# Kernel optimization log

Measured on AMD Instinct MI355X. Metric: run time of the kernel, lower is better.

## Reference

```python
import jax, jax.numpy as jnp
import numpy as np

B, S, D, H = 4, 2048, 1024, 16
DH = D // H  # 64


def setup_inputs() -> dict:
    key = jax.random.key(0)
    ks = jax.random.split(key, 11)
    s = 0.02
    return {
        "query": jax.random.normal(ks[0], (B, S, D), jnp.float32),
        "key": jax.random.normal(ks[1], (B, S, D), jnp.float32),
        "value": jax.random.normal(ks[2], (B, S, D), jnp.float32),
        "Wq": jax.random.normal(ks[3], (D, D), jnp.float32) * s,
        "bq": jnp.zeros((D,), jnp.float32),
        "Wk": jax.random.normal(ks[4], (D, D), jnp.float32) * s,
        "bk": jnp.zeros((D,), jnp.float32),
        "Wv": jax.random.normal(ks[5], (D, D), jnp.float32) * s,
        "bv": jnp.zeros((D,), jnp.float32),
        "Wo": jax.random.normal(ks[6], (D, D), jnp.float32) * s,
        "bo": jnp.zeros((D,), jnp.float32),
    }


def reference(query, key, value, Wq, bq, Wk, bk, Wv, bv, Wo, bo):
    b, s, _ = query.shape
    # linear projections (torch Linear: x @ W^T + b; here W stored as [in, out])
    q = query @ Wq + bq
    k = key @ Wk + bk
    v = value @ Wv + bv
    # split heads -> [B, H, S, DH]
    q = q.reshape(b, s, H, DH).transpose(0, 2, 1, 3)
    k = k.reshape(b, s, H, DH).transpose(0, 2, 1, 3)
    v = v.reshape(b, s, H, DH).transpose(0, 2, 1, 3)
    scale = jnp.sqrt(jnp.asarray(DH, jnp.float32))
    attn = jnp.einsum("bhqd,bhkd->bhqk", q, k) / scale  # [B,H,S,S]
    attn = jax.nn.softmax(attn, axis=-1)
    out = jnp.einsum("bhqk,bhkd->bhqd", attn, v)
    out = out.transpose(0, 2, 1, 3).reshape(b, s, D)
    return out @ Wo + bo
```

## Files before the change

kernel.cpp:

```cpp
#include <hip/hip_runtime.h>

typedef float f32x4 __attribute__((ext_vector_type(4)));
typedef __bf16 bf16x8 __attribute__((ext_vector_type(8)));
typedef unsigned short u16;
typedef unsigned int u32;
typedef u16 u16x4 __attribute__((ext_vector_type(4)));
typedef u16 u16x8 __attribute__((ext_vector_type(8)));
typedef u32 u32x2 __attribute__((ext_vector_type(2)));
typedef u32 u32x4 __attribute__((ext_vector_type(4)));

constexpr int Bn = 4, Sn = 2048, Dn = 1024, Hn = 16, DHn = 64;
constexpr int Mn = Bn * Sn;

static __device__ __forceinline__ u16 f2bf(float f) {
  return __builtin_bit_cast(u16, (__bf16)f);
}

static __device__ __forceinline__ u32 cvtpk(float lo, float hi) {
  u32 r;
  asm("v_cvt_pk_bf16_f32 %0, %1, %2" : "=v"(r) : "v"(lo), "v"(hi));
  return r;
}

static __device__ __forceinline__ void async16(const void* g, void* l) {
  __builtin_amdgcn_global_load_lds((const __attribute__((address_space(1))) u32*)g,
                                   (__attribute__((address_space(3))) u32*)l, 16, 0, 0);
}

static __device__ __forceinline__ void wait_bar2() {
  asm volatile("s_waitcnt vmcnt(2)" ::: "memory");
  __builtin_amdgcn_sched_barrier(0);
  __builtin_amdgcn_s_barrier();
  __builtin_amdgcn_sched_barrier(0);
}
static __device__ __forceinline__ void wait_bar0() {
  asm volatile("s_waitcnt vmcnt(0)" ::: "memory");
  __builtin_amdgcn_sched_barrier(0);
  __builtin_amdgcn_s_barrier();
  __builtin_amdgcn_sched_barrier(0);
}
static __device__ __forceinline__ void wait_bar8() {
  asm volatile("s_waitcnt vmcnt(8)" ::: "memory");
  __builtin_amdgcn_sched_barrier(0);
  __builtin_amdgcn_s_barrier();
  __builtin_amdgcn_sched_barrier(0);
}
static __device__ __forceinline__ void raw_bar() {
  __builtin_amdgcn_sched_barrier(0);
  __builtin_amdgcn_s_barrier();
  __builtin_amdgcn_sched_barrier(0);
}

__global__ void __launch_bounds__(256) cvt3_kernel(const float* __restrict__ q,
                                                   const float* __restrict__ k,
                                                   const float* __restrict__ v,
                                                   u16* __restrict__ dst) {
  const int i = blockIdx.x * 256 + threadIdx.x;
  const int t = i >> 20;
  const int li = i & 1048575;
  const float* s = (t == 0) ? q : (t == 1) ? k : v;
  const f32x4* sp = (const f32x4*)s + (size_t)li * 2;
  const f32x4 a = sp[0], b = sp[1];
  u16x8 o;
  o[0] = f2bf(a[0]); o[1] = f2bf(a[1]); o[2] = f2bf(a[2]); o[3] = f2bf(a[3]);
  o[4] = f2bf(b[0]); o[5] = f2bf(b[1]); o[6] = f2bf(b[2]); o[7] = f2bf(b[3]);
  ((u16x8*)dst)[i] = o;
}

__global__ void __launch_bounds__(256) transpose_w_kernel(const float* __restrict__ W,
                                                          u16* __restrict__ Wt) {
  __shared__ float tile[32][33];
  const int n0 = blockIdx.x * 32, k0 = blockIdx.y * 32;
  const int tx = threadIdx.x & 31, ty = (threadIdx.x >> 5) * 4;
#pragma unroll
  for (int i = 0; i < 4; ++i)
    tile[ty + i][tx] = W[(size_t)(k0 + ty + i) * Dn + n0 + tx];
  __syncthreads();
#pragma unroll
  for (int i = 0; i < 4; ++i)
    Wt[(size_t)(n0 + ty + i) * Dn + k0 + tx] = f2bf(tile[tx][ty + i]);
}

template <int MODE>
__global__ void __launch_bounds__(256) gemm_kernel(const u16* __restrict__ A,
                                                   const u16* __restrict__ Bt,
                                                   const float* __restrict__ bias,
                                                   void* __restrict__ outp, float scale) {
  __shared__ u16 As[2][128 * 64];
  __shared__ u16 Bs[2][128 * 64];
  const int tid = threadIdx.x;
  const int wave = tid >> 6, lane = tid & 63;
  const int g = lane >> 4, c = lane & 15;
  const int m0 = blockIdx.y * 128, n0 = blockIdx.x * 128;
  const int wm = wave >> 1, wn = wave & 1;
  const int srow = lane >> 3, blk = lane & 7;

  f32x4 acc[4][4] = {};
  constexpr int NK = Dn / 64;

#pragma unroll
  for (int p = 0; p < 2; ++p) {
    const int k0 = p * 64;
#pragma unroll
    for (int i = 0; i < 4; ++i) {
      const int ch = wave * 4 + i;
      const int row = ch * 8 + srow;
      const int sblk = blk ^ srow;
      async16(A + (size_t)(m0 + row) * Dn + k0 + sblk * 8, As[p] + ch * 512);
      async16(Bt + (size_t)(n0 + row) * Dn + k0 + sblk * 8, Bs[p] + ch * 512);
    }
  }

  for (int k = 0; k < NK; ++k) {
    const int cur = k & 1;
    if (k + 1 < NK) wait_bar8(); else wait_bar0();

#pragma unroll
    for (int kk = 0; kk < 2; ++kk) {
      bf16x8 af[4], bfr[4];
#pragma unroll
      for (int mi = 0; mi < 4; ++mi)
        af[mi] = *(const bf16x8*)(As[cur] + (wm * 64 + mi * 16 + c) * 64 +
                                  (((kk * 4 + g) ^ (c & 7)) * 8));
#pragma unroll
      for (int ni = 0; ni < 4; ++ni)
        bfr[ni] = *(const bf16x8*)(Bs[cur] + (wn * 64 + ni * 16 + c) * 64 +
                                   (((kk * 4 + g) ^ (c & 7)) * 8));
#pragma unroll
      for (int mi = 0; mi < 4; ++mi)
#pragma unroll
        for (int ni = 0; ni < 4; ++ni)
          acc[mi][ni] = __builtin_amdgcn_mfma_f32_16x16x32_bf16(af[mi], bfr[ni],
                                                                acc[mi][ni], 0, 0, 0);
    }

    raw_bar();
    if (k + 2 < NK) {
      const int k0 = (k + 2) * 64;
#pragma unroll
      for (int i = 0; i < 4; ++i) {
        const int ch = wave * 4 + i;
        const int row = ch * 8 + srow;
        const int sblk = blk ^ srow;
        async16(A + (size_t)(m0 + row) * Dn + k0 + sblk * 8, As[cur] + ch * 512);
        async16(Bt + (size_t)(n0 + row) * Dn + k0 + sblk * 8, Bs[cur] + ch * 512);
      }
    }
  }

#pragma unroll
  for (int ni = 0; ni < 4; ++ni) {
    const int col = n0 + wn * 64 + ni * 16 + c;
    const float bv = bias[col];
#pragma unroll
    for (int mi = 0; mi < 4; ++mi) {
      const int row = m0 + wm * 64 + mi * 16 + g * 4;
      if constexpr (MODE == 0) {
        const int hh = col >> 6, dh = col & 63;
        const int bb = row >> 11, s = row & 2047;
        u16* o = (u16*)outp + (((size_t)(bb * Hn + hh) * Sn + s) * DHn + dh);
#pragma unroll
        for (int r = 0; r < 4; ++r)
          o[(size_t)r * DHn] = f2bf((acc[mi][ni][r] + bv) * scale);
      } else if constexpr (MODE == 1) {
        const int hh = col >> 6, dh = col & 63;
        const int bb = row >> 11, s = row & 2047;
        u16x4 pk;
#pragma unroll
        for (int r = 0; r < 4; ++r) pk[r] = f2bf(acc[mi][ni][r] + bv);
        *(u16x4*)((u16*)outp + ((size_t)(bb * Hn + hh) * DHn + dh) * Sn + s) = pk;
      } else {
        float* o = (float*)outp + (size_t)row * Dn + col;
#pragma unroll
        for (int r = 0; r < 4; ++r) o[(size_t)r * Dn] = acc[mi][ni][r] + bv;
      }
    }
  }
}

__global__ void __launch_bounds__(512, 4) attn_kernel(const u16* __restrict__ Q,
                                                      const u16* __restrict__ Kp,
                                                      const u16* __restrict__ VT,
                                                      u16* __restrict__ O) {
  __shared__ u16 Ks[3][64 * 64];
  __shared__ u16 Vs[3][64 * 64];
  const int tid = threadIdx.x;
  const int wave = tid >> 6, lane = tid & 63;
  const int g = lane >> 4, c = lane & 15;
  const int bh = blockIdx.x;
  const int q0 = blockIdx.y * 256 + wave * 32;
  const u16* Qb = Q + (size_t)bh * Sn * DHn;
  const u16* Kb = Kp + (size_t)bh * Sn * DHn;
  const u16* Vb = VT + (size_t)bh * DHn * Sn;

  bf16x8 qf[2][2];
#pragma unroll
  for (int fq = 0; fq < 2; ++fq)
#pragma unroll
    for (int kk = 0; kk < 2; ++kk)
      qf[fq][kk] = *(const bf16x8*)(Qb + (size_t)(q0 + fq * 16 + c) * DHn + kk * 32 + g * 8);

  f32x4 ot[4][2] = {};
  f32x4 lacc[2] = {};
  u16x8 one8u;
#pragma unroll
  for (int j = 0; j < 8; ++j) one8u[j] = 0x3F80;
  const bf16x8 one8 = __builtin_bit_cast(bf16x8, one8u);
  const f32x4 zf = {};

  const int srow = lane >> 3, blk = lane & 7;
  const int krow = wave * 8 + srow;
  const int sblk = blk ^ srow;
  constexpr int NT = Sn / 64;

  u16 *kA = Ks[0], *kB = Ks[1], *kC = Ks[2];
  u16 *vA = Vs[0], *vB = Vs[1], *vC = Vs[2];

#pragma unroll
  for (int tt = 0; tt < 2; ++tt) {
    const int kt = tt * 64;
    async16(Kb + (size_t)(kt + krow) * DHn + sblk * 8, Ks[tt] + wave * 512);
    async16(Vb + (size_t)krow * Sn + kt + sblk * 8, Vs[tt] + wave * 512);
  }

  for (int t = 0; t < NT; ++t) {
    if (t + 1 < NT) wait_bar2(); else wait_bar0();

    if (t + 2 < NT) {
      const int kt = (t + 2) * 64;
      async16(Kb + (size_t)(kt + krow) * DHn + sblk * 8, kC + wave * 512);
      async16(Vb + (size_t)krow * Sn + kt + sblk * 8, vC + wave * 512);
    }

    f32x4 st[4][2];
    {
      bf16x8 kf[4];
#pragma unroll
      for (int fk = 0; fk < 4; ++fk)
        kf[fk] = *(const bf16x8*)(kA + (fk * 16 + c) * 64 + ((g ^ (c & 7)) * 8));
      __builtin_amdgcn_s_setprio(1);
#pragma unroll
      for (int fk = 0; fk < 4; ++fk)
#pragma unroll
        for (int fq = 0; fq < 2; ++fq)
          st[fk][fq] = __builtin_amdgcn_mfma_f32_16x16x32_bf16(kf[fk], qf[fq][0],
                                                               zf, 0, 0, 0);
      __builtin_amdgcn_s_setprio(0);
#pragma unroll
      for (int fk = 0; fk < 4; ++fk)
        kf[fk] = *(const bf16x8*)(kA + (fk * 16 + c) * 64 + (((4 + g) ^ (c & 7)) * 8));
      __builtin_amdgcn_s_setprio(1);
#pragma unroll
      for (int fk = 0; fk < 4; ++fk)
#pragma unroll
        for (int fq = 0; fq < 2; ++fq)
          st[fk][fq] = __builtin_amdgcn_mfma_f32_16x16x32_bf16(kf[fk], qf[fq][1],
                                                               st[fk][fq], 0, 0, 0);
      __builtin_amdgcn_s_setprio(0);
    }

#pragma unroll
    for (int fq = 0; fq < 2; ++fq)
#pragma unroll
      for (int fk = 0; fk < 4; ++fk)
#pragma unroll
        for (int r = 0; r < 4; ++r)
          st[fk][fq][r] = __builtin_amdgcn_exp2f(st[fk][fq][r]);

    bf16x8 pf[2][2];
#pragma unroll
    for (int fq = 0; fq < 2; ++fq)
#pragma unroll
      for (int kk = 0; kk < 2; ++kk) {
        u32x4 pw;
#pragma unroll
        for (int w = 0; w < 2; ++w) {
          const u32 a = cvtpk(st[2 * kk][fq][2 * w], st[2 * kk][fq][2 * w + 1]);
          const u32 b = cvtpk(st[2 * kk + 1][fq][2 * w], st[2 * kk + 1][fq][2 * w + 1]);
          const u32x2 p1 = __builtin_amdgcn_permlane32_swap(a, b, false, false);
          const u32x2 p2 = __builtin_amdgcn_permlane16_swap(p1[0], p1[1], false, false);
          pw[w] = p2[0];
          pw[2 + w] = p2[1];
        }
        pf[kk][fq] = __builtin_bit_cast(bf16x8, pw);
      }

#pragma unroll
    for (int kk = 0; kk < 2; ++kk) {
      bf16x8 vf[4];
#pragma unroll
      for (int fa = 0; fa < 4; ++fa)
        vf[fa] = *(const bf16x8*)(vA + (fa * 16 + c) * 64 +
                                  (((kk * 4 + g) ^ (c & 7)) * 8));
      __builtin_amdgcn_s_setprio(1);
#pragma unroll
      for (int fa = 0; fa < 4; ++fa)
#pragma unroll
        for (int fq = 0; fq < 2; ++fq)
          ot[fa][fq] = __builtin_amdgcn_mfma_f32_16x16x32_bf16(vf[fa], pf[kk][fq],
                                                               ot[fa][fq], 0, 0, 0);
#pragma unroll
      for (int fq = 0; fq < 2; ++fq)
        lacc[fq] = __builtin_amdgcn_mfma_f32_16x16x32_bf16(one8, pf[kk][fq],
                                                           lacc[fq], 0, 0, 0);
      __builtin_amdgcn_s_setprio(0);
    }

    u16* tk = kA; kA = kB; kB = kC; kC = tk;
    u16* tv = vA; vA = vB; vB = vC; vC = tv;
  }

  const int bb = bh >> 4, hh = bh & 15;
#pragma unroll
  for (int fq = 0; fq < 2; ++fq) {
    const float inv = 1.f / lacc[fq][0];
    const int s = q0 + fq * 16 + c;
#pragma unroll
    for (int fa = 0; fa < 4; ++fa) {
      const int dh = fa * 16 + g * 4;
      u16x4 pk;
#pragma unroll
      for (int r = 0; r < 4; ++r) pk[r] = f2bf(ot[fa][fq][r] * inv);
      *(u16x4*)(O + ((size_t)bb * Sn + s) * Dn + hh * 64 + dh) = pk;
    }
  }
}

extern "C" void kernel_launch(void* const* d_in, const int* in_sizes, int n_in,
                              void* d_out, int out_size, void* d_ws, size_t ws_size,
                              hipStream_t stream) {
  (void)in_sizes; (void)n_in; (void)out_size; (void)ws_size;
  const float* q_in = (const float*)d_in[0];
  const float* k_in = (const float*)d_in[1];
  const float* v_in = (const float*)d_in[2];
  const float* Wq = (const float*)d_in[3];
  const float* bq = (const float*)d_in[4];
  const float* Wk = (const float*)d_in[5];
  const float* bk = (const float*)d_in[6];
  const float* Wv = (const float*)d_in[7];
  const float* bv = (const float*)d_in[8];
  const float* Wo = (const float*)d_in[9];
  const float* bo = (const float*)d_in[10];

  char* ws = (char*)d_ws;
  const size_t szX = (size_t)Mn * Dn * 2;
  const size_t szW = (size_t)Dn * Dn * 2;
  u16* Xq = (u16*)(ws + 0 * szX);
  u16* Xk = (u16*)(ws + 1 * szX);
  u16* Xv = (u16*)(ws + 2 * szX);
  u16* Wqt = (u16*)(ws + 3 * szX + 0 * szW);
  u16* Wkt = (u16*)(ws + 3 * szX + 1 * szW);
  u16* Wvt = (u16*)(ws + 3 * szX + 2 * szW);
  u16* Wot = (u16*)(ws + 3 * szX + 3 * szW);
  u16* Qb = (u16*)(ws + 3 * szX + 4 * szW + 0 * szX);
  u16* Kb = (u16*)(ws + 3 * szX + 4 * szW + 1 * szX);
  u16* VTb = (u16*)(ws + 3 * szX + 4 * szW + 2 * szX);
  u16* Ob = (u16*)(ws + 3 * szX + 4 * szW + 3 * szX);

  cvt3_kernel<<<3 * Mn * Dn / 8 / 256, 256, 0, stream>>>(q_in, k_in, v_in, Xq);

  dim3 tg(32, 32);
  transpose_w_kernel<<<tg, 256, 0, stream>>>(Wq, Wqt);
  transpose_w_kernel<<<tg, 256, 0, stream>>>(Wk, Wkt);
  transpose_w_kernel<<<tg, 256, 0, stream>>>(Wv, Wvt);
  transpose_w_kernel<<<tg, 256, 0, stream>>>(Wo, Wot);

  dim3 gg(Dn / 128, Mn / 128);
  const float qscale = 0.125f * 1.4426950408889634f;
  gemm_kernel<0><<<gg, 256, 0, stream>>>(Xq, Wqt, bq, Qb, qscale);
  gemm_kernel<0><<<gg, 256, 0, stream>>>(Xk, Wkt, bk, Kb, 1.0f);
  gemm_kernel<1><<<gg, 256, 0, stream>>>(Xv, Wvt, bv, VTb, 1.0f);

  attn_kernel<<<dim3(Bn * Hn, Sn / 256), 512, 0, stream>>>(Qb, Kb, VTb, Ob);

  gemm_kernel<2><<<gg, 256, 0, stream>>>(Ob, Wot, bo, d_out, 1.0f);
}
```

Baseline: 204.4 us.

## Fuse fp32-to-bf16 input conversion into batched QKV GEMM; merge weight transposes

Removes the separate cvt3 kernel that wrote bf16 copies of query/key/value. The QKV GEMM now loads fp32 activations into registers, converts them to bf16 and writes them to LDS, while B tiles still arrive via async global-to-LDS loads. The three projection GEMMs and the four weight transposes are each merged into one launch using blockIdx.z. This saves a full bf16 round trip through memory and several launches, but the GEMM now reads twice as many activation bytes and uses register-staged A loads, which may hurt overlap.

```diff
diff --git a/kernel.cpp b/kernel.cpp
--- a/kernel.cpp
+++ b/kernel.cpp
@@ -33,43 +33,45 @@
   __builtin_amdgcn_s_barrier();
   __builtin_amdgcn_sched_barrier(0);
 }
+static __device__ __forceinline__ void wait_bar4() {
+  asm volatile("s_waitcnt vmcnt(4)" ::: "memory");
+  __builtin_amdgcn_sched_barrier(0);
+  __builtin_amdgcn_s_barrier();
+  __builtin_amdgcn_sched_barrier(0);
+}
+static __device__ __forceinline__ void wait_bar8() {
+  asm volatile("s_waitcnt vmcnt(8)" ::: "memory");
+  __builtin_amdgcn_sched_barrier(0);
+  __builtin_amdgcn_s_barrier();
+  __builtin_amdgcn_sched_barrier(0);
+}
 static __device__ __forceinline__ void wait_bar0() {
   asm volatile("s_waitcnt vmcnt(0)" ::: "memory");
   __builtin_amdgcn_sched_barrier(0);
   __builtin_amdgcn_s_barrier();
   __builtin_amdgcn_sched_barrier(0);
 }
-static __device__ __forceinline__ void wait_bar8() {
-  asm volatile("s_waitcnt vmcnt(8)" ::: "memory");
-  __builtin_amdgcn_sched_barrier(0);
-  __builtin_amdgcn_s_barrier();
-  __builtin_amdgcn_sched_barrier(0);
-}
 static __device__ __forceinline__ void raw_bar() {
   __builtin_amdgcn_sched_barrier(0);
   __builtin_amdgcn_s_barrier();
   __builtin_amdgcn_sched_barrier(0);
 }
-
-__global__ void __launch_bounds__(256) cvt3_kernel(const float* __restrict__ q,
-                                                   const float* __restrict__ k,
-                                                   const float* __restrict__ v,
-                                                   u16* __restrict__ dst) {
-  const int i = blockIdx.x * 256 + threadIdx.x;
-  const int t = i >> 20;
-  const int li = i & 1048575;
-  const float* s = (t == 0) ? q : (t == 1) ? k : v;
-  const f32x4* sp = (const f32x4*)s + (size_t)li * 2;
-  const f32x4 a = sp[0], b = sp[1];
-  u16x8 o;
-  o[0] = f2bf(a[0]); o[1] = f2bf(a[1]); o[2] = f2bf(a[2]); o[3] = f2bf(a[3]);
-  o[4] = f2bf(b[0]); o[5] = f2bf(b[1]); o[6] = f2bf(b[2]); o[7] = f2bf(b[3]);
-  ((u16x8*)dst)[i] = o;
-}
-
-__global__ void __launch_bounds__(256) transpose_w_kernel(const float* __restrict__ W,
-                                                          u16* __restrict__ Wt) {
+static __device__ __forceinline__ void lgkm_bar() {
+  asm volatile("s_waitcnt lgkmcnt(0)" ::: "memory");
+  __builtin_amdgcn_sched_barrier(0);
+  __builtin_amdgcn_s_barrier();
+  __builtin_amdgcn_sched_barrier(0);
+}
+
+__global__ void __launch_bounds__(256) transpose4_kernel(const float* __restrict__ Wq,
+                                                         const float* __restrict__ Wk,
+                                                         const float* __restrict__ Wv,
+                                                         const float* __restrict__ Wo,
+                                                         u16* __restrict__ Wts) {
   __shared__ float tile[32][33];
+  const int z = blockIdx.z;
+  const float* W = (z == 0) ? Wq : (z == 1) ? Wk : (z == 2) ? Wv : Wo;
+  u16* Wt = Wts + (size_t)z * Dn * Dn;
   const int n0 = blockIdx.x * 32, k0 = blockIdx.y * 32;
   const int tx = threadIdx.x & 31, ty = (threadIdx.x >> 5) * 4;
 #pragma unroll
@@ -81,11 +83,135 @@
     Wt[(size_t)(n0 + ty + i) * Dn + k0 + tx] = f2bf(tile[tx][ty + i]);
 }
 
-template <int MODE>
-__global__ void __launch_bounds__(256) gemm_kernel(const u16* __restrict__ A,
-                                                   const u16* __restrict__ Bt,
-                                                   const float* __restrict__ bias,
-                                                   void* __restrict__ outp, float scale) {
+__global__ void __launch_bounds__(256) gemm_qkv_kernel(const float* __restrict__ q_in,
+                                                       const float* __restrict__ k_in,
+                                                       const float* __restrict__ v_in,
+                                                       const u16* __restrict__ Wts,
+                                                       const float* __restrict__ bq,
+                                                       const float* __restrict__ bk,
+                                                       const float* __restrict__ bv,
+                                                       u16* __restrict__ outbase) {
+  __shared__ u16 As[2][128 * 64];
+  __shared__ u16 Bs[2][128 * 64];
+  const int z = blockIdx.z;
+  const float* A = (z == 0) ? q_in : (z == 1) ? k_in : v_in;
+  const u16* Bt = Wts + (size_t)z * Dn * Dn;
+  const float* bias = (z == 0) ? bq : (z == 1) ? bk : bv;
+  u16* outp = outbase + (size_t)z * Mn * Dn;
+  const float scale = (z == 0) ? 0.125f * 1.4426950408889634f : 1.0f;
+
+  const int tid = threadIdx.x;
+  const int wave = tid >> 6, lane = tid & 63;
+  const int g = lane >> 4, c = lane & 15;
+  const int m0 = blockIdx.y * 128, n0 = blockIdx.x * 128;
+  const int wm = wave >> 1, wn = wave & 1;
+  const int srow = lane >> 3, blk = lane & 7;
+
+  f32x4 acc[4][4] = {};
+  constexpr int NK = Dn / 64;
+
+  f32x4 ralo[4], rahi[4];
+
+  auto issueA = [&](int k0) {
+#pragma unroll
+    for (int i = 0; i < 4; ++i) {
+      const int row = (wave * 4 + i) * 8 + srow;
+      const float* src = A + (size_t)(m0 + row) * Dn + k0 + blk * 8;
+      ralo[i] = *(const f32x4*)src;
+      rahi[i] = *(const f32x4*)(src + 4);
+    }
+  };
+  auto writeA = [&](u16* dst) {
+#pragma unroll
+    for (int i = 0; i < 4; ++i) {
+      const int row = (wave * 4 + i) * 8 + srow;
+      u32x4 w;
+      w[0] = cvtpk(ralo[i][0], ralo[i][1]);
+      w[1] = cvtpk(ralo[i][2], ralo[i][3]);
+      w[2] = cvtpk(rahi[i][0], rahi[i][1]);
+      w[3] = cvtpk(rahi[i][2], rahi[i][3]);
+      *(u32x4*)(dst + row * 64 + ((blk ^ srow) * 8)) = w;
+    }
+  };
+  auto issueB = [&](int k0, u16* dstB) {
+#pragma unroll
+    for (int i = 0; i < 4; ++i) {
+      const int ch = wave * 4 + i, row = ch * 8 + srow, sb = blk ^ srow;
+      async16(Bt + (size_t)(n0 + row) * Dn + k0 + sb * 8, dstB + ch * 512);
+    }
+  };
+
+  issueA(0);
+  issueB(0, Bs[0]);
+  asm volatile("s_waitcnt vmcnt(4)" ::: "memory");
+  __builtin_amdgcn_sched_barrier(0);
+  writeA(As[0]);
+  issueA(64);
+  issueB(64, Bs[1]);
+  asm volatile("s_waitcnt lgkmcnt(0)" ::: "memory");
+  __builtin_amdgcn_sched_barrier(0);
+
+  for (int k = 0; k < NK; ++k) {
+    const int cur = k & 1;
+    if (k + 1 < NK) wait_bar4(); else wait_bar0();
+
+    if (k + 1 < NK) writeA(As[cur ^ 1]);
+
+#pragma unroll
+    for (int kk = 0; kk < 2; ++kk) {
+      bf16x8 af[4], bfr[4];
+#pragma unroll
+      for (int mi = 0; mi < 4; ++mi)
+        af[mi] = *(const bf16x8*)(As[cur] + (wm * 64 + mi * 16 + c) * 64 +
+                                  (((kk * 4 + g) ^ (c & 7)) * 8));
+#pragma unroll
+      for (int ni = 0; ni < 4; ++ni)
+        bfr[ni] = *(const bf16x8*)(Bs[cur] + (wn * 64 + ni * 16 + c) * 64 +
+                                   (((kk * 4 + g) ^ (c & 7)) * 8));
+#pragma unroll
+      for (int mi = 0; mi < 4; ++mi)
+#pragma unroll
+        for (int ni = 0; ni < 4; ++ni)
+          acc[mi][ni] = __builtin_amdgcn_mfma_f32_16x16x32_bf16(af[mi], bfr[ni],
+                                                                acc[mi][ni], 0, 0, 0);
+    }
+
+    lgkm_bar();
+    if (k + 2 < NK) {
+      issueA((k + 2) * 64);
+      issueB((k + 2) * 64, Bs[cur]);
+    }
+  }
+
+  const bool vmode = (z == 2);
+#pragma unroll
+  for (int ni = 0; ni < 4; ++ni) {
+    const int col = n0 + wn * 64 + ni * 16 + c;
+    const float bv = bias[col];
+    const int hh = col >> 6, dh = col & 63;
+#pragma unroll
+    for (int mi = 0; mi < 4; ++mi) {
+      const int row = m0 + wm * 64 + mi * 16 + g * 4;
+      const int bb = row >> 11, s = row & 2047;
+      if (!vmode) {
+        u16* o = outp + (((size_t)(bb * Hn + hh) * Sn + s) * DHn + dh);
+#pragma unroll
+        for (int r = 0; r < 4; ++r)
+          o[(size_t)r * DHn] = f2bf((acc[mi][ni][r] + bv) * scale);
+      } else {
+        u16x4 pk;
+#pragma unroll
+        for (int r = 0; r < 4; ++r) pk[r] = f2bf(acc[mi][ni][r] + bv);
+        *(u16x4*)(outp + ((size_t)(bb * Hn + hh) * DHn + dh) * Sn + s) = pk;
+      }
+    }
+  }
+}
+
+__global__ void __launch_bounds__(256) gemm_o_kernel(const u16* __restrict__ A,
+                                                     const u16* __restrict__ Bt,
+                                                     const float* __restrict__ bias,
+                                                     float* __restrict__ outp) {
   __shared__ u16 As[2][128 * 64];
   __shared__ u16 Bs[2][128 * 64];
   const int tid = threadIdx.x;
@@ -155,25 +281,9 @@
 #pragma unroll
     for (int mi = 0; mi < 4; ++mi) {
       const int row = m0 + wm * 64 + mi * 16 + g * 4;
-      if constexpr (MODE == 0) {
-        const int hh = col >> 6, dh = col & 63;
-        const int bb = row >> 11, s = row & 2047;
-        u16* o = (u16*)outp + (((size_t)(bb * Hn + hh) * Sn + s) * DHn + dh);
-#pragma unroll
-        for (int r = 0; r < 4; ++r)
-          o[(size_t)r * DHn] = f2bf((acc[mi][ni][r] + bv) * scale);
-      } else if constexpr (MODE == 1) {
-        const int hh = col >> 6, dh = col & 63;
-        const int bb = row >> 11, s = row & 2047;
-        u16x4 pk;
-#pragma unroll
-        for (int r = 0; r < 4; ++r) pk[r] = f2bf(acc[mi][ni][r] + bv);
-        *(u16x4*)((u16*)outp + ((size_t)(bb * Hn + hh) * DHn + dh) * Sn + s) = pk;
-      } else {
-        float* o = (float*)outp + (size_t)row * Dn + col;
-#pragma unroll
-        for (int r = 0; r < 4; ++r) o[(size_t)r * Dn] = acc[mi][ni][r] + bv;
-      }
+      float* o = outp + (size_t)row * Dn + col;
+#pragma unroll
+      for (int r = 0; r < 4; ++r) o[(size_t)r * Dn] = acc[mi][ni][r] + bv;
     }
   }
 }
@@ -345,33 +455,19 @@
   char* ws = (char*)d_ws;
   const size_t szX = (size_t)Mn * Dn * 2;
   const size_t szW = (size_t)Dn * Dn * 2;
-  u16* Xq = (u16*)(ws + 0 * szX);
-  u16* Xk = (u16*)(ws + 1 * szX);
-  u16* Xv = (u16*)(ws + 2 * szX);
-  u16* Wqt = (u16*)(ws + 3 * szX + 0 * szW);
-  u16* Wkt = (u16*)(ws + 3 * szX + 1 * szW);
-  u16* Wvt = (u16*)(ws + 3 * szX + 2 * szW);
-  u16* Wot = (u16*)(ws + 3 * szX + 3 * szW);
-  u16* Qb = (u16*)(ws + 3 * szX + 4 * szW + 0 * szX);
-  u16* Kb = (u16*)(ws + 3 * szX + 4 * szW + 1 * szX);
-  u16* VTb = (u16*)(ws + 3 * szX + 4 * szW + 2 * szX);
-  u16* Ob = (u16*)(ws + 3 * szX + 4 * szW + 3 * szX);
-
-  cvt3_kernel<<<3 * Mn * Dn / 8 / 256, 256, 0, stream>>>(q_in, k_in, v_in, Xq);
-
-  dim3 tg(32, 32);
-  transpose_w_kernel<<<tg, 256, 0, stream>>>(Wq, Wqt);
-  transpose_w_kernel<<<tg, 256, 0, stream>>>(Wk, Wkt);
-  transpose_w_kernel<<<tg, 256, 0, stream>>>(Wv, Wvt);
-  transpose_w_kernel<<<tg, 256, 0, stream>>>(Wo, Wot);
-
-  dim3 gg(Dn / 128, Mn / 128);
-  const float qscale = 0.125f * 1.4426950408889634f;
-  gemm_kernel<0><<<gg, 256, 0, stream>>>(Xq, Wqt, bq, Qb, qscale);
-  gemm_kernel<0><<<gg, 256, 0, stream>>>(Xk, Wkt, bk, Kb, 1.0f);
-  gemm_kernel<1><<<gg, 256, 0, stream>>>(Xv, Wvt, bv, VTb, 1.0f);
+  u16* Wts = (u16*)ws;
+  u16* Qb = (u16*)(ws + 4 * szW + 0 * szX);
+  u16* Kb = (u16*)(ws + 4 * szW + 1 * szX);
+  u16* VTb = (u16*)(ws + 4 * szW + 2 * szX);
+  u16* Ob = (u16*)(ws + 4 * szW + 3 * szX);
+
+  transpose4_kernel<<<dim3(32, 32, 4), 256, 0, stream>>>(Wq, Wk, Wv, Wo, Wts);
+
+  gemm_qkv_kernel<<<dim3(Dn / 128, Mn / 128, 3), 256, 0, stream>>>(
+      q_in, k_in, v_in, Wts, bq, bk, bv, Qb);
 
   attn_kernel<<<dim3(Bn * Hn, Sn / 256), 512, 0, stream>>>(Qb, Kb, VTb, Ob);
 
-  gemm_kernel<2><<<gg, 256, 0, stream>>>(Ob, Wot, bo, d_out, 1.0f);
-}
+  gemm_o_kernel<<<dim3(Dn / 128, Mn / 128), 256, 0, stream>>>(
+      Ob, Wts + (size_t)3 * Dn * Dn, bo, (float*)d_out);
+}
```

Result: slower. 222.3 us (+8.8%).
